# Kernel optimization log

Measured on AMD Instinct MI355X. Metric: run time of the kernel, lower is better.

Reference implementation:

```python
import jax, jax.numpy as jnp
import numpy as np

N_BITS = 8
P_LO, P_HI = 0.01, 0.02
REDUCE = (0, 2, 3)  # is_conv=True
Q_MAX = float(2 ** N_BITS - 1)  # get_bounds(n_bits, signed=False) -> (0, 2^n - 1)


def setup_inputs() -> dict:
    key = jax.random.key(0)
    # Unsigned (post-ReLU) activations with range > 1 so the bisection iterates.
    x = jax.random.uniform(key, (16, 128, 112, 112), dtype=jnp.float32) * 16.0
    return {"x": x}


def _percent_bound(x):
    """Per-channel binary search for a threshold `upper` such that the fraction
    of elements above it lies in [P_LO, P_HI] (or the bracket shrinks to <= 1)."""
    size = x.shape[0] * x.shape[2] * x.shape[3]
    max_val = jnp.max(x, axis=REDUCE, keepdims=True)  # [1, C, 1, 1]
    left = jnp.zeros_like(max_val)
    right = max_val

    def frac_above(pivot):
        return jnp.sum((x > pivot).astype(jnp.float32), axis=REDUCE, keepdims=True) / size

    def cond_fn(state):
        l, r = state
        per = frac_above((l + r) * 0.5)
        ok = jnp.logical_or(
            jnp.logical_and(P_LO <= per, per <= P_HI),
            (r - l) <= 1.0,
        )
        return jnp.logical_not(jnp.all(ok))

    def body_fn(state):
        l, r = state
        pivot = (l + r) * 0.5
        per = frac_above(pivot)
        l2 = jnp.where(per > P_HI, pivot, l)
        r2 = jnp.where(per < P_LO, pivot, r)
        return (l2, r2)

    l, r = jax.lax.while_loop(cond_fn, body_fn, (left, right))
    return (l + r) * 0.5  # pivot at break time, matching the torch loop


def reference(x):
    # Training-mode forward. Binary search is non-differentiable bookkeeping
    # (bisection over comparisons), so the shift is a stop-gradient quantity.
    upper = jax.lax.stop_gradient(_percent_bound(x))  # [1, C, 1, 1]
    cur_shift = N_BITS - jnp.log2(upper)
    r_shift = jnp.round(cur_shift)  # STERound (shift already stop-grad)
    scaled = x * jnp.exp2(r_shift)
    # STEFloor: floor in fwd, identity in bwd
    q = scaled + jax.lax.stop_gradient(jnp.floor(scaled) - scaled)
    return jnp.clip(q, 0.0, Q_MAX)
```

## Files before the change

kernel.cpp:

```cpp
#include <hip/hip_runtime.h>
#include <stdint.h>

#define CHW   12544
#define NSLAB 2048
#define NCH   128
#define NBINS 2048
#define NGRP  4
#define BINSCALE 128.0f
#define SIZE_PER_C 200704.0f
#define QMAXV 255.0f

typedef float vf4 __attribute__((ext_vector_type(4)));

__global__ __launch_bounds__(256) void kstats(const float* __restrict__ x,
                                              unsigned* __restrict__ hist_part,
                                              float* __restrict__ max_part) {
    __shared__ unsigned h[NBINS];
    __shared__ float sm[4];
    int c = blockIdx.x & (NCH - 1);
    int g = blockIdx.x >> 7;
    int t = threadIdx.x;
    for (int i = t; i < NBINS; i += 256) h[i] = 0u;
    __syncthreads();
    float m = 0.0f;
    for (int n = g * 4; n < g * 4 + 4; ++n) {
        const float4* p = (const float4*)(x + (size_t)(n * NCH + c) * CHW);
        for (int i = t; i < CHW / 4; i += 256) {
            float4 v = p[i];
            m = fmaxf(m, fmaxf(fmaxf(v.x, v.y), fmaxf(v.z, v.w)));
            atomicAdd(&h[min(NBINS - 1, (int)(v.x * BINSCALE))], 1u);
            atomicAdd(&h[min(NBINS - 1, (int)(v.y * BINSCALE))], 1u);
            atomicAdd(&h[min(NBINS - 1, (int)(v.z * BINSCALE))], 1u);
            atomicAdd(&h[min(NBINS - 1, (int)(v.w * BINSCALE))], 1u);
        }
    }
    for (int off = 32; off > 0; off >>= 1)
        m = fmaxf(m, __shfl_down(m, off));
    if ((t & 63) == 0) sm[t >> 6] = m;
    __syncthreads();
    if (t == 0)
        max_part[blockIdx.x] = fmaxf(fmaxf(sm[0], sm[1]), fmaxf(sm[2], sm[3]));
    unsigned* hp = hist_part + (size_t)((c << 2) + g) * NBINS;
    for (int i = t; i < NBINS; i += 256) hp[i] = h[i];
}

__global__ __launch_bounds__(256) void ksuffix(const unsigned* __restrict__ hist_part,
                                               const float* __restrict__ max_part,
                                               unsigned* __restrict__ suf,
                                               float* __restrict__ chanmax) {
    __shared__ unsigned chunk[256];
    int c = blockIdx.x;
    int t = threadIdx.x;
    int base = t * 8;
    unsigned v[8] = {0, 0, 0, 0, 0, 0, 0, 0};
    #pragma unroll
    for (int g = 0; g < NGRP; ++g) {
        const uint4* q = (const uint4*)(hist_part + (size_t)((c << 2) + g) * NBINS + base);
        uint4 a = q[0], b = q[1];
        v[0] += a.x; v[1] += a.y; v[2] += a.z; v[3] += a.w;
        v[4] += b.x; v[5] += b.y; v[6] += b.z; v[7] += b.w;
    }
    unsigned s = 0;
    #pragma unroll
    for (int j = 7; j >= 0; --j) s += v[j];
    chunk[t] = s;
    __syncthreads();
    for (int off = 1; off < 256; off <<= 1) {
        unsigned add = (t + off < 256) ? chunk[t + off] : 0u;
        __syncthreads();
        chunk[t] += add;
        __syncthreads();
    }
    unsigned tail = (t < 255) ? chunk[t + 1] : 0u;
    unsigned* sc = suf + (size_t)c * (NBINS + 1);
    unsigned w = tail;
    #pragma unroll
    for (int j = 7; j >= 0; --j) {
        w += v[j];
        sc[base + j] = w;
    }
    if (t == 255) sc[NBINS] = 0u;
    if (t == 0) {
        const float* mp = max_part + (c << 2);
        chanmax[c] = fmaxf(fmaxf(mp[0], mp[1]), fmaxf(mp[2], mp[3]));
    }
}

__global__ void kbisect(const float* __restrict__ chanmax,
                        const unsigned* __restrict__ suf,
                        float* __restrict__ scale) {
    int c = threadIdx.x;
    float maxv = chanmax[c];
    const unsigned* sc = suf + (size_t)c * (NBINS + 1);
    float l = 0.0f, r = maxv;
    __shared__ int nok;
    float upper = 0.5f * maxv;
    for (int iter = 0; iter < 64; ++iter) {
        float pivot = (l + r) * 0.5f;
        int e = (int)roundf(pivot * BINSCALE);
        e = e < 0 ? 0 : (e > NBINS ? NBINS : e);
        unsigned cnt = sc[e];
        float per = (float)cnt / SIZE_PER_C;
        bool ok = (per >= 0.01f && per <= 0.02f) || (r - l) <= 1.0f;
        if (threadIdx.x == 0) nok = 0;
        __syncthreads();
        if (!ok) atomicAdd(&nok, 1);
        __syncthreads();
        if (nok == 0) { upper = pivot; break; }
        if (per > 0.02f) l = pivot;
        else if (per < 0.01f) r = pivot;
        upper = (l + r) * 0.5f;
        __syncthreads();
    }
    float cur_shift = 8.0f - log2f(upper);
    float r_shift = rintf(cur_shift);
    scale[c] = exp2f(r_shift);
}

__global__ __launch_bounds__(256) void kquant(const float* __restrict__ x,
                                              const float* __restrict__ scale,
                                              float* __restrict__ out) {
    int slab = blockIdx.x;
    int c = slab & (NCH - 1);
    float s = scale[c];
    const float4* p = (const float4*)(x + (size_t)slab * CHW);
    vf4* q = (vf4*)(out + (size_t)slab * CHW);
    for (int i = threadIdx.x; i < CHW / 4; i += 256) {
        float4 v = p[i];
        vf4 r;
        r.x = fminf(fmaxf(floorf(v.x * s), 0.0f), QMAXV);
        r.y = fminf(fmaxf(floorf(v.y * s), 0.0f), QMAXV);
        r.z = fminf(fmaxf(floorf(v.z * s), 0.0f), QMAXV);
        r.w = fminf(fmaxf(floorf(v.w * s), 0.0f), QMAXV);
        __builtin_nontemporal_store(r, &q[i]);
    }
}

extern "C" void kernel_launch(void* const* d_in, const int* in_sizes, int n_in,
                              void* d_out, int out_size, void* d_ws, size_t ws_size,
                              hipStream_t stream) {
    const float* x = (const float*)d_in[0];
    float* out = (float*)d_out;

    unsigned* hist_part = (unsigned*)d_ws;
    unsigned* suf       = hist_part + (size_t)NCH * NGRP * NBINS;
    float*    max_part  = (float*)(suf + (size_t)NCH * (NBINS + 1));
    float*    chanmax   = max_part + NCH * NGRP;
    float*    scale     = chanmax + NCH;

    kstats <<<NCH * NGRP, 256, 0, stream>>>(x, hist_part, max_part);
    ksuffix<<<NCH, 256, 0, stream>>>(hist_part, max_part, suf, chanmax);
    kbisect<<<1, NCH, 0, stream>>>(chanmax, suf, scale);
    kquant <<<NSLAB, 256, 0, stream>>>(x, scale, out);
}
```

Baseline: 66.61 us.

## Fuse suffix-sum and bisection into one kernel, double histogram partitions

Merges the suffix-scan and bisection kernels into a single per-channel kernel that keeps the suffix array in shared memory and runs the bisection on one thread per channel, removing a launch and the global suffix buffer round-trip. The histogram stage is split into 8 groups per channel instead of 4, doubling block count for better occupancy at the cost of more partial histogram writes and reads.

New measurement: 58.67 us. 11.9% less time.

```diff
diff --git a/kernel.cpp b/kernel.cpp
--- a/kernel.cpp
+++ b/kernel.cpp
@@ -5,7 +5,7 @@
 #define NSLAB 2048
 #define NCH   128
 #define NBINS 2048
-#define NGRP  4
+#define NGRP  8
 #define BINSCALE 128.0f
 #define SIZE_PER_C 200704.0f
 #define QMAXV 255.0f
@@ -23,7 +23,7 @@
     for (int i = t; i < NBINS; i += 256) h[i] = 0u;
     __syncthreads();
     float m = 0.0f;
-    for (int n = g * 4; n < g * 4 + 4; ++n) {
+    for (int n = g * 2; n < g * 2 + 2; ++n) {
         const float4* p = (const float4*)(x + (size_t)(n * NCH + c) * CHW);
         for (int i = t; i < CHW / 4; i += 256) {
             float4 v = p[i];
@@ -39,15 +39,15 @@
     if ((t & 63) == 0) sm[t >> 6] = m;
     __syncthreads();
     if (t == 0)
-        max_part[blockIdx.x] = fmaxf(fmaxf(sm[0], sm[1]), fmaxf(sm[2], sm[3]));
-    unsigned* hp = hist_part + (size_t)((c << 2) + g) * NBINS;
+        max_part[(c << 3) + g] = fmaxf(fmaxf(sm[0], sm[1]), fmaxf(sm[2], sm[3]));
+    unsigned* hp = hist_part + (size_t)((c << 3) + g) * NBINS;
     for (int i = t; i < NBINS; i += 256) hp[i] = h[i];
 }
 
-__global__ __launch_bounds__(256) void ksuffix(const unsigned* __restrict__ hist_part,
-                                               const float* __restrict__ max_part,
-                                               unsigned* __restrict__ suf,
-                                               float* __restrict__ chanmax) {
+__global__ __launch_bounds__(256) void kscale(const unsigned* __restrict__ hist_part,
+                                              const float* __restrict__ max_part,
+                                              float* __restrict__ scale) {
+    __shared__ unsigned suf[NBINS];
     __shared__ unsigned chunk[256];
     int c = blockIdx.x;
     int t = threadIdx.x;
@@ -55,7 +55,7 @@
     unsigned v[8] = {0, 0, 0, 0, 0, 0, 0, 0};
     #pragma unroll
     for (int g = 0; g < NGRP; ++g) {
-        const uint4* q = (const uint4*)(hist_part + (size_t)((c << 2) + g) * NBINS + base);
+        const uint4* q = (const uint4*)(hist_part + (size_t)((c << 3) + g) * NBINS + base);
         uint4 a = q[0], b = q[1];
         v[0] += a.x; v[1] += a.y; v[2] += a.z; v[3] += a.w;
         v[4] += b.x; v[5] += b.y; v[6] += b.z; v[7] += b.w;
@@ -72,49 +72,36 @@
         __syncthreads();
     }
     unsigned tail = (t < 255) ? chunk[t + 1] : 0u;
-    unsigned* sc = suf + (size_t)c * (NBINS + 1);
     unsigned w = tail;
     #pragma unroll
     for (int j = 7; j >= 0; --j) {
         w += v[j];
-        sc[base + j] = w;
+        suf[base + j] = w;
     }
-    if (t == 255) sc[NBINS] = 0u;
+    __syncthreads();
     if (t == 0) {
-        const float* mp = max_part + (c << 2);
-        chanmax[c] = fmaxf(fmaxf(mp[0], mp[1]), fmaxf(mp[2], mp[3]));
+        const float* mp = max_part + (c << 3);
+        float maxv = mp[0];
+        #pragma unroll
+        for (int g = 1; g < NGRP; ++g) maxv = fmaxf(maxv, mp[g]);
+        float l = 0.0f, r = maxv;
+        float upper = 0.5f * maxv;
+        for (int iter = 0; iter < 64; ++iter) {
+            float pivot = (l + r) * 0.5f;
+            int e = (int)roundf(pivot * BINSCALE);
+            e = e < 0 ? 0 : (e > NBINS ? NBINS : e);
+            unsigned cnt = (e < NBINS) ? suf[e] : 0u;
+            float per = (float)cnt / SIZE_PER_C;
+            bool ok = (per >= 0.01f && per <= 0.02f) || (r - l) <= 1.0f;
+            if (ok) { upper = pivot; break; }
+            if (per > 0.02f) l = pivot;
+            else if (per < 0.01f) r = pivot;
+            upper = (l + r) * 0.5f;
+        }
+        float cur_shift = 8.0f - log2f(upper);
+        float r_shift = rintf(cur_shift);
+        scale[c] = exp2f(r_shift);
     }
-}
-
-__global__ void kbisect(const float* __restrict__ chanmax,
-                        const unsigned* __restrict__ suf,
-                        float* __restrict__ scale) {
-    int c = threadIdx.x;
-    float maxv = chanmax[c];
-    const unsigned* sc = suf + (size_t)c * (NBINS + 1);
-    float l = 0.0f, r = maxv;
-    __shared__ int nok;
-    float upper = 0.5f * maxv;
-    for (int iter = 0; iter < 64; ++iter) {
-        float pivot = (l + r) * 0.5f;
-        int e = (int)roundf(pivot * BINSCALE);
-        e = e < 0 ? 0 : (e > NBINS ? NBINS : e);
-        unsigned cnt = sc[e];
-        float per = (float)cnt / SIZE_PER_C;
-        bool ok = (per >= 0.01f && per <= 0.02f) || (r - l) <= 1.0f;
-        if (threadIdx.x == 0) nok = 0;
-        __syncthreads();
-        if (!ok) atomicAdd(&nok, 1);
-        __syncthreads();
-        if (nok == 0) { upper = pivot; break; }
-        if (per > 0.02f) l = pivot;
-        else if (per < 0.01f) r = pivot;
-        upper = (l + r) * 0.5f;
-        __syncthreads();
-    }
-    float cur_shift = 8.0f - log2f(upper);
-    float r_shift = rintf(cur_shift);
-    scale[c] = exp2f(r_shift);
 }
 
 __global__ __launch_bounds__(256) void kquant(const float* __restrict__ x,
@@ -143,13 +130,10 @@
     float* out = (float*)d_out;
 
     unsigned* hist_part = (unsigned*)d_ws;
-    unsigned* suf       = hist_part + (size_t)NCH * NGRP * NBINS;
-    float*    max_part  = (float*)(suf + (size_t)NCH * (NBINS + 1));
-    float*    chanmax   = max_part + NCH * NGRP;
-    float*    scale     = chanmax + NCH;
+    float*    max_part  = (float*)(hist_part + (size_t)NCH * NGRP * NBINS);
+    float*    scale     = max_part + NCH * NGRP;
 
     kstats <<<NCH * NGRP, 256, 0, stream>>>(x, hist_part, max_part);
-    ksuffix<<<NCH, 256, 0, stream>>>(hist_part, max_part, suf, chanmax);
-    kbisect<<<1, NCH, 0, stream>>>(chanmax, suf, scale);
+    kscale <<<NCH, 256, 0, stream>>>(hist_part, max_part, scale);
     kquant <<<NSLAB, 256, 0, stream>>>(x, scale, out);
 }
```
